# Optimization experiments

Hardware: AMD Instinct MI355X
Metric: run time of the kernel (lower is better)

Reference implementation:

```python
import jax, jax.numpy as jnp
import numpy as np

# ---- dims (match init_kwargs) ----
B0, C0, H0, W0 = 16, 64, 128, 128
G = 8            # d_model of inner Mamba2
D_STATE = 16
D_CONV = 3
EXPAND = 2
HEADDIM = 8
D_INNER = EXPAND * G            # 16
NHEADS = D_INNER // HEADDIM     # 2
NGROUPS = 1
CONV_DIM = D_INNER + 2 * NGROUPS * D_STATE   # 48
D_IN_PROJ = 2 * D_INNER + 2 * NGROUPS * D_STATE + NHEADS  # 66
EPS = 1e-5


def silu(x):
    return x * jax.nn.sigmoid(x)


def setup_inputs() -> dict:
    key = jax.random.key(0)
    ks = jax.random.split(key, 12)
    s = 0.02
    return {
        "x": jax.random.normal(ks[0], (B0, C0, H0, W0), jnp.float32),
        # 1x1 conv tokenize / detokenize (stored as matrices)
        "w_tok": jax.random.normal(ks[1], (G, C0), jnp.float32) * s,
        "b_tok": jnp.zeros((G,), jnp.float32),
        "w_detok": jax.random.normal(ks[2], (C0, G), jnp.float32) * s,
        "b_detok": jnp.zeros((C0,), jnp.float32),
        # Mamba2 params
        "w_in": jax.random.normal(ks[3], (D_IN_PROJ, G), jnp.float32) * s,
        "w_conv": jax.random.normal(ks[4], (CONV_DIM, 1, D_CONV), jnp.float32) * s,
        "b_conv": jnp.zeros((CONV_DIM,), jnp.float32),
        "dt_bias": jax.random.uniform(ks[5], (NHEADS,), jnp.float32, -4.0, -2.0),
        "A_log": jnp.log(jnp.arange(1, NHEADS + 1, dtype=jnp.float32)),
        "D": jnp.ones((NHEADS,), jnp.float32),
        "norm_w": jnp.ones((D_INNER,), jnp.float32),
        "w_out": jax.random.normal(ks[6], (G, D_INNER), jnp.float32) * s,
    }


def _mamba2(u, w_in, w_conv, b_conv, dt_bias, A_log, D, norm_w, w_out):
    # u: [B, L, G]
    Bb, L, _ = u.shape
    zxbcdt = jnp.einsum('blg,dg->bld', u, w_in)                 # [B,L,66]
    z = zxbcdt[..., :D_INNER]                                   # [B,L,16]
    xBC = zxbcdt[..., D_INNER:D_INNER + CONV_DIM]               # [B,L,48]
    dt = jax.nn.softplus(zxbcdt[..., D_INNER + CONV_DIM:] + dt_bias)  # [B,L,H]

    # causal depthwise conv1d over time
    xBC_t = jnp.moveaxis(xBC, 1, 2)                             # [B,48,L]
    xBC_t = jnp.pad(xBC_t, ((0, 0), (0, 0), (D_CONV - 1, 0)))
    xBC_t = jax.lax.conv_general_dilated(
        xBC_t, w_conv, window_strides=(1,), padding='VALID',
        dimension_numbers=('NCH', 'OIH', 'NCH'), feature_group_count=CONV_DIM)
    xBC = silu(jnp.moveaxis(xBC_t + b_conv[None, :, None], 1, 2))  # [B,L,48]

    xh = xBC[..., :D_INNER].reshape(Bb, L, NHEADS, HEADDIM)     # [B,L,H,P]
    Bm = xBC[..., D_INNER:D_INNER + D_STATE]                    # [B,L,N] (ngroups=1)
    Cm = xBC[..., D_INNER + D_STATE:]                           # [B,L,N]

    A = -jnp.exp(A_log)                                         # [H]
    dA = jnp.exp(dt * A)                                        # [B,L,H]

    # time-major sequential selective scan
    def step(state, inp):
        dA_t, dt_t, x_t, B_t, C_t = inp  # [B,H],[B,H],[B,H,P],[B,N],[B,N]
        state = state * dA_t[:, :, None, None] \
            + (dt_t[:, :, None] * x_t)[..., None] * B_t[:, None, None, :]
        y = jnp.einsum('bhpn,bn->bhp', state, C_t)
        return state, y

    init = jnp.zeros((Bb, NHEADS, HEADDIM, D_STATE), u.dtype)
    xs = (jnp.moveaxis(dA, 1, 0), jnp.moveaxis(dt, 1, 0),
          jnp.moveaxis(xh, 1, 0), jnp.moveaxis(Bm, 1, 0), jnp.moveaxis(Cm, 1, 0))
    _, ys = jax.lax.scan(step, init, xs)                        # [L,B,H,P]
    y = jnp.moveaxis(ys, 0, 1) + D[None, None, :, None] * xh    # [B,L,H,P]
    y = y.reshape(Bb, L, D_INNER)

    # gated RMSNorm then out projection
    y = y * silu(z)
    y = y * jax.lax.rsqrt(jnp.mean(y * y, axis=-1, keepdims=True) + EPS) * norm_w
    return jnp.einsum('bld,gd->blg', y, w_out)


def reference(x, w_tok, b_tok, w_detok, b_detok, w_in, w_conv, b_conv,
              dt_bias, A_log, D, norm_w, w_out):
    Bb, C, H, W = x.shape
    g = jnp.einsum('bchw,gc->bghw', x, w_tok) + b_tok[None, :, None, None]
    g = g.reshape(Bb, G, H * W).transpose(0, 2, 1)              # [B,HW,G]
    g = _mamba2(g, w_in, w_conv, b_conv, dt_bias, A_log, D, norm_w, w_out) + g
    g = g.transpose(0, 2, 1).reshape(Bb, G, H, W)
    return x + jnp.einsum('bghw,cg->bchw', g, w_detok) + b_detok[None, :, None, None]
```

## Files before the change

kernel.cpp:

```cpp
#include <hip/hip_runtime.h>

namespace {
constexpr int NB   = 16;
constexpr int NC   = 64;
constexpr int HW   = 128*128;
constexpr int SL   = 16384;
constexpr int CQ   = 64;
constexpr int NCH  = SL/CQ;
constexpr int WCH  = 4;

typedef short short8 __attribute__((ext_vector_type(8)));
typedef float f32x4  __attribute__((ext_vector_type(4)));

__device__ __forceinline__ float frcp(float x){ return __builtin_amdgcn_rcpf(x); }
__device__ __forceinline__ float rl(float v, int s){
  return __int_as_float(__builtin_amdgcn_readlane(__float_as_int(v), s));
}
__device__ __forceinline__ float sigu(float a){ return frcp(1.0f + __expf(-a)); }
__device__ __forceinline__ float softplusf(float a){
  return fmaxf(a, 0.f) + __logf(1.f + __expf(-fabsf(a)));
}
__device__ __forceinline__ unsigned bfr(float x){
  unsigned u = __float_as_uint(x);
  u = u + 0x7FFF + ((u>>16)&1);
  return u>>16;
}
__device__ __forceinline__ unsigned pk2(float a, float b){
  return (bfr(a)&0xFFFFu) | (bfr(b)<<16);
}
union CV8 { unsigned u[4]; short8 s; };

__global__ __launch_bounds__(256) void k_tok(
    const float* __restrict__ x, const float* __restrict__ w_tok,
    const float* __restrict__ b_tok, float* __restrict__ g0)
{
  __shared__ float s_wt[NC][8];
  __shared__ float s_bt[8];
  for (int i = threadIdx.x; i < NC*8; i += 256) s_wt[i>>3][i&7] = w_tok[(i&7)*NC + (i>>3)];
  if (threadIdx.x < 8) s_bt[threadIdx.x] = b_tok[threadIdx.x];
  __syncthreads();
  long idx = (long)blockIdx.x * 256 + threadIdx.x;
  int b = (int)(idx >> 14);
  int l = (int)(idx & (SL-1));
  float acc[8];
  #pragma unroll
  for (int g = 0; g < 8; ++g) acc[g] = s_bt[g];
  const float* xp = x + (long)b*NC*HW + l;
  #pragma unroll 8
  for (int c = 0; c < NC; ++c) {
    float v = xp[(long)c*HW];
    const float4* wr = (const float4*)s_wt[c];
    float4 w0 = wr[0], w1 = wr[1];
    acc[0] += v*w0.x; acc[1] += v*w0.y; acc[2] += v*w0.z; acc[3] += v*w0.w;
    acc[4] += v*w1.x; acc[5] += v*w1.y; acc[6] += v*w1.z; acc[7] += v*w1.w;
  }
  float* gp = g0 + idx*8;
  *(float4*)gp     = make_float4(acc[0],acc[1],acc[2],acc[3]);
  *(float4*)(gp+4) = make_float4(acc[4],acc[5],acc[6],acc[7]);
}

template<int PASS>
__global__ __launch_bounds__(256)
void k_chunk(
    const float* __restrict__ g0, const float* __restrict__ w_in,
    const float* __restrict__ w_conv, const float* __restrict__ b_conv,
    const float* __restrict__ dt_bias, const float* __restrict__ A_log,
    const float* __restrict__ Dvec, const float* __restrict__ norm_w,
    const float* __restrict__ w_out,
    float* __restrict__ Sc, float* __restrict__ Pc,
    const float* __restrict__ Stin, float* __restrict__ gf)
{
  constexpr int JMAX = (PASS==1) ? 48 : 32;
  constexpr int PW = (PASS==1) ? 10752 : 4096;
  __shared__ float s_win[66][8];
  __shared__ float s_wc[48][4];
  __shared__ float s_wout[8][16];
  __shared__ float s_nw[16];
  __shared__ float s_misc[8];
  __shared__ char  s_big[WCH*PW];

  int tid = threadIdx.x, lane = tid & 63, wave = tid >> 6;
  int c15 = lane & 15, lg = lane >> 4;

  for (int i = tid; i < 66*8; i += 256) s_win[i>>3][i&7] = w_in[i];
  if (tid < 48) {
    s_wc[tid][0] = w_conv[tid*3];   s_wc[tid][1] = w_conv[tid*3+1];
    s_wc[tid][2] = w_conv[tid*3+2]; s_wc[tid][3] = b_conv[tid];
  }
  if (tid < 128) s_wout[tid>>4][tid&15] = w_out[tid];
  if (tid < 16)  s_nw[tid] = norm_w[tid];
  if (tid < 2) {
    s_misc[tid]   = -__expf(A_log[tid]);
    s_misc[2+tid] = dt_bias[tid];
    s_misc[4+tid] = Dvec[tid];
  }
  __syncthreads();

  auto dot8 = [&](const float* uu, int row) -> float {
    const float4* wr = (const float4*)s_win[row];
    float4 w0 = wr[0], w1 = wr[1];
    return uu[0]*w0.x + uu[1]*w0.y + uu[2]*w0.z + uu[3]*w0.w
         + uu[4]*w1.x + uu[5]*w1.y + uu[6]*w1.z + uu[7]*w1.w;
  };

  int b   = blockIdx.x >> 6;
  int chB = (blockIdx.x & 63)*WCH + wave;
  long cg = (long)b*NCH + chB;
  int l0  = chB*CQ;
  long pos = (long)b*SL + l0 + lane;
  char* WR = &s_big[wave*PW];

  float u[8];
  { const float* up = g0 + pos*8;
    float4 a = *(const float4*)up, c = *(const float4*)(up+4);
    u[0]=a.x;u[1]=a.y;u[2]=a.z;u[3]=a.w;u[4]=c.x;u[5]=c.y;u[6]=c.z;u[7]=c.w; }

  float hA, hB = 0.f;
  {
    int pA = lane >> 5, jA = lane & 31;
    int hlA = l0 - 2 + pA;
    bool okA = (hlA >= 0);
    const float* hp2 = g0 + ((long)b*SL + (okA ? hlA : 0))*8;
    float4 a = *(const float4*)hp2, c = *(const float4*)(hp2+4);
    float uA[8] = {a.x,a.y,a.z,a.w,c.x,c.y,c.z,c.w};
    hA = okA ? dot8(uA, 16+jA) : 0.f;
    if constexpr (PASS==1) {
      int pB = (lane >> 4) & 1, jB = 32 + (lane & 15);
      int hlB = l0 - 2 + pB;
      bool okB = (hlB >= 0);
      const float* hq = g0 + ((long)b*SL + (okB ? hlB : 0))*8;
      float4 a2 = *(const float4*)hq, c2 = *(const float4*)(hq+4);
      float uB[8] = {a2.x,a2.y,a2.z,a2.w,c2.x,c2.y,c2.z,c2.w};
      hB = okB ? dot8(uB, 16+jB) : 0.f;
    }
  }

  float xv[16], Bv[16];
  float Cr[(PASS==1) ? 16 : 1];
  #pragma unroll
  for (int jb = 0; jb < JMAX/8; ++jb) {
    float pr[8];
    #pragma unroll
    for (int jj = 0; jj < 8; ++jj) pr[jj] = dot8(u, 16 + jb*8 + jj);
    #pragma unroll
    for (int jj = 0; jj < 8; ++jj) {
      int j = jb*8 + jj;
      float pm1 = __shfl_up(pr[jj], 1);
      float pm2 = __shfl_up(pr[jj], 2);
      float h0j = (j < 32) ? rl(hA, j)      : rl(hB, j-32);
      float h1j = (j < 32) ? rl(hA, 32+j)   : rl(hB, 16+(j-32));
      pm1 = (lane == 0) ? h1j : pm1;
      pm2 = (lane == 0) ? h0j : ((lane == 1) ? h1j : pm2);
      float4 wc = *(const float4*)s_wc[j];
      float a = wc.w + pm2*wc.x + pm1*wc.y + pr[jj]*wc.z;
      float s = a * sigu(a);
      if (j < 16) xv[j] = s;
      else if (j < 32) Bv[j-16] = s;
      else { if constexpr (PASS==1) Cr[j-32] = s; }
    }
  }

  float dt0 = softplusf(dot8(u, 64) + s_misc[2]);
  float dt1 = softplusf(dot8(u, 65) + s_misc[3]);
  float c0 = s_misc[0]*dt0, c1 = s_misc[1]*dt1;
  #pragma unroll
  for (int off = 1; off < 64; off <<= 1) {
    float t0 = __shfl_up(c0, off), t1 = __shfl_up(c1, off);
    if (lane >= off) { c0 += t0; c1 += t1; }
  }
  float ce0 = __expf(c0), ce1 = __expf(c1);
  float cf0 = __expf(-c0)*dt0, cf1 = __expf(-c1)*dt1;
  float cee0 = rl(ce0, 63), cee1 = rl(ce1, 63);

  char* xp = WR + ((PASS==1) ? 8192 : 2048);
  #pragma unroll
  for (int hp = 0; hp < 16; ++hp) {
    float cfh = (hp < 8) ? cf0 : cf1;
    *(short*)(xp + hp*128 + ((lane*2) ^ ((hp&7)<<4))) = (short)bfr(cfh*xv[hp]);
  }

  if constexpr (PASS==0) {
    char* BT = WR;
    #pragma unroll
    for (int n = 0; n < 16; ++n)
      *(short*)(BT + n*128 + ((lane*2) ^ ((n&7)<<4))) = (short)bfr(Bv[n]);
    __builtin_amdgcn_wave_barrier();
    __builtin_amdgcn_sched_barrier(0);
    f32x4 acc = {0.f,0.f,0.f,0.f};
    #pragma unroll
    for (int kb = 0; kb < 2; ++kb) {
      int cb = (64*kb + 16*lg) ^ ((c15&7)<<4);
      short8 Af = *(const short8*)(xp + c15*128 + cb);
      short8 Bf = *(const short8*)(BT + c15*128 + cb);
      acc = __builtin_amdgcn_mfma_f32_16x16x32_bf16(Af, Bf, acc, 0, 0, 0);
    }
    float cee = (lg < 2) ? cee0 : cee1;
    #pragma unroll
    for (int r = 0; r < 4; ++r)
      Sc[cg*256 + (4*lg+r)*16 + c15] = cee*acc[r];
    if (lane == 0) { Pc[cg*2] = cee0; Pc[cg*2+1] = cee1; }
  } else {
    char* uB  = WR;
    char* uC  = WR + 2048;
    char* Mb  = WR;
    char* ytr = WR;
    char* ceB = WR + 10240;
    { CV8 w;
      w.u[0]=pk2(Bv[0],Bv[1]);  w.u[1]=pk2(Bv[2],Bv[3]);
      w.u[2]=pk2(Bv[4],Bv[5]);  w.u[3]=pk2(Bv[6],Bv[7]);
      *(short8*)(uB + lane*32) = w.s;
      w.u[0]=pk2(Bv[8],Bv[9]);  w.u[1]=pk2(Bv[10],Bv[11]);
      w.u[2]=pk2(Bv[12],Bv[13]);w.u[3]=pk2(Bv[14],Bv[15]);
      *(short8*)(uB + lane*32 + 16) = w.s;
      w.u[0]=pk2(Cr[0],Cr[1]);  w.u[1]=pk2(Cr[2],Cr[3]);
      w.u[2]=pk2(Cr[4],Cr[5]);  w.u[3]=pk2(Cr[6],Cr[7]);
      *(short8*)(uC + lane*32) = w.s;
      w.u[0]=pk2(Cr[8],Cr[9]);  w.u[1]=pk2(Cr[10],Cr[11]);
      w.u[2]=pk2(Cr[12],Cr[13]);w.u[3]=pk2(Cr[14],Cr[15]);
      *(short8*)(uC + lane*32 + 16) = w.s;
    }
    *(float*)(ceB + lane*4)       = ce0;
    *(float*)(ceB + 256 + lane*4) = ce1;
    __builtin_amdgcn_wave_barrier();
    __builtin_amdgcn_sched_barrier(0);

    short8 zero8 = {0,0,0,0,0,0,0,0};
    f32x4  zero4 = {0.f,0.f,0.f,0.f};
    short8 Cfr[4], Bfr[4];
    #pragma unroll
    for (int tt = 0; tt < 4; ++tt) {
      Cfr[tt] = zero8; Bfr[tt] = zero8;
      if (lg < 2) {
        Cfr[tt] = *(const short8*)(uC + (16*tt + c15)*32 + 16*lg);
        Bfr[tt] = *(const short8*)(uB + (16*tt + c15)*32 + 16*lg);
      }
    }
    short8 stf = zero8;
    if (lg < 2) {
      const float* sp = Stin + cg*256 + c15*16 + 8*lg;
      float4 s0 = *(const float4*)sp, s1 = *(const float4*)(sp+4);
      CV8 cv;
      cv.u[0]=pk2(s0.x,s0.y); cv.u[1]=pk2(s0.z,s0.w);
      cv.u[2]=pk2(s1.x,s1.y); cv.u[3]=pk2(s1.z,s1.w);
      stf = cv.s;
    }
    f32x4 acc[4];
    #pragma unroll
    for (int tt = 0; tt < 4; ++tt)
      acc[tt] = __builtin_amdgcn_mfma_f32_16x16x32_bf16(Cfr[tt], stf, zero4, 0,0,0);

    #pragma unroll
    for (int tt = 0; tt < 4; ++tt) {
      int t  = 16*tt + c15;
      int sw = (t&7)<<4;
      #pragma unroll
      for (int ts = 0; ts < 4; ++ts) {
        if (ts <= tt) {
          f32x4 gA = __builtin_amdgcn_mfma_f32_16x16x32_bf16(Bfr[ts], Cfr[tt], zero4, 0,0,0);
          if (ts == tt) {
            #pragma unroll
            for (int r = 0; r < 4; ++r)
              gA[r] = (4*lg + r <= c15) ? gA[r] : 0.f;
          }
          uint2 wv; wv.x = pk2(gA[0],gA[1]); wv.y = pk2(gA[2],gA[3]);
          *(uint2*)(Mb + t*128 + ((32*ts + 8*lg) ^ sw)) = wv;
        }
      }
      if (tt == 0 || tt == 2) {
        uint2 zv; zv.x = 0u; zv.y = 0u;
        *(uint2*)(Mb + t*128 + ((32*(tt+1) + 8*lg) ^ sw)) = zv;
      }
    }
    __builtin_amdgcn_wave_barrier();
    __builtin_amdgcn_sched_barrier(0);

    short8 Xf[2];
    #pragma unroll
    for (int kb = 0; kb < 2; ++kb)
      Xf[kb] = *(const short8*)(xp + c15*128 + ((64*kb + 16*lg) ^ ((c15&7)<<4)));
    #pragma unroll
    for (int tt = 0; tt < 4; ++tt) {
      int t = 16*tt + c15, sw = (t&7)<<4;
      {
        short8 Mf = *(const short8*)(Mb + t*128 + ((16*lg) ^ sw));
        acc[tt] = __builtin_amdgcn_mfma_f32_16x16x32_bf16(Mf, Xf[0], acc[tt], 0,0,0);
      }
      if (tt >= 2) {
        short8 Mf = *(const short8*)(Mb + t*128 + ((64 + 16*lg) ^ sw));
        acc[tt] = __builtin_amdgcn_mfma_f32_16x16x32_bf16(Mf, Xf[1], acc[tt], 0,0,0);
      }
    }
    int hh = (c15 < 8) ? 0 : 1;
    #pragma unroll
    for (int tt = 0; tt < 4; ++tt) {
      float4 cev = *(const float4*)(ceB + hh*256 + (16*tt + 4*lg)*4);
      float cva[4] = {cev.x, cev.y, cev.z, cev.w};
      #pragma unroll
      for (int r = 0; r < 4; ++r)
        *(float*)(ytr + (16*tt + 4*lg + r)*96 + c15*4) = cva[r]*acc[tt][r];
    }
    __builtin_amdgcn_wave_barrier();
    __builtin_amdgcn_sched_barrier(0);

    float yr[16];
    #pragma unroll
    for (int i = 0; i < 4; ++i) {
      float4 q = *(const float4*)(ytr + lane*96 + 16*i);
      yr[4*i] = q.x; yr[4*i+1] = q.y; yr[4*i+2] = q.z; yr[4*i+3] = q.w;
    }
    float D0 = s_misc[4], D1 = s_misc[5];
    float yv[16]; float ss = 0.f;
    #pragma unroll
    for (int d = 0; d < 16; ++d) {
      float base = yr[d] + ((d < 8) ? D0 : D1)*xv[d];
      float zz = dot8(u, d);
      float v = base * (zz * sigu(zz));
      yv[d] = v; ss += v*v;
    }
    float scn = rsqrtf(ss*(1.f/16.f) + 1e-5f);
    { const float4* nw = (const float4*)s_nw;
      float4 n0 = nw[0], n1 = nw[1], n2 = nw[2], n3 = nw[3];
      yv[0]*=scn*n0.x; yv[1]*=scn*n0.y; yv[2]*=scn*n0.z; yv[3]*=scn*n0.w;
      yv[4]*=scn*n1.x; yv[5]*=scn*n1.y; yv[6]*=scn*n1.z; yv[7]*=scn*n1.w;
      yv[8]*=scn*n2.x; yv[9]*=scn*n2.y; yv[10]*=scn*n2.z; yv[11]*=scn*n2.w;
      yv[12]*=scn*n3.x; yv[13]*=scn*n3.y; yv[14]*=scn*n3.z; yv[15]*=scn*n3.w; }
    float og[8];
    #pragma unroll
    for (int g = 0; g < 8; ++g) {
      const float4* wr = (const float4*)s_wout[g];
      float4 w0 = wr[0], w1 = wr[1], w2 = wr[2], w3 = wr[3];
      float a = u[g];
      a += yv[0]*w0.x + yv[1]*w0.y + yv[2]*w0.z + yv[3]*w0.w;
      a += yv[4]*w1.x + yv[5]*w1.y + yv[6]*w1.z + yv[7]*w1.w;
      a += yv[8]*w2.x + yv[9]*w2.y + yv[10]*w2.z + yv[11]*w2.w;
      a += yv[12]*w3.x + yv[13]*w3.y + yv[14]*w3.z + yv[15]*w3.w;
      og[g] = a;
    }
    float* gp = gf + pos*8;
    *(float4*)gp     = make_float4(og[0],og[1],og[2],og[3]);
    *(float4*)(gp+4) = make_float4(og[4],og[5],og[6],og[7]);
  }
}

__global__ __launch_bounds__(256) void k_scan(
    const float* __restrict__ Sc, const float* __restrict__ Pc,
    float* __restrict__ Stin)
{
  int b = blockIdx.x;
  int tid = threadIdx.x;
  int h = tid >> 7;
  float st = 0.f;
  long base = (long)b * NCH;
  #pragma unroll 8
  for (int c = 0; c < NCH; ++c) {
    Stin[(base + c)*256 + tid] = st;
    st = st * Pc[(base + c)*2 + h] + Sc[(base + c)*256 + tid];
  }
}

__global__ __launch_bounds__(256) void k_detok(
    const float* __restrict__ x, const float* __restrict__ gf,
    const float* __restrict__ w_detok, const float* __restrict__ b_detok,
    float* __restrict__ out)
{
  __shared__ float s_wd[NC][8];
  __shared__ float s_bd[NC];
  for (int i = threadIdx.x; i < NC*8; i += 256) s_wd[i>>3][i&7] = w_detok[i];
  if (threadIdx.x < NC) s_bd[threadIdx.x] = b_detok[threadIdx.x];
  __syncthreads();
  long idx = (long)blockIdx.x * 256 + threadIdx.x;
  int b = (int)(idx >> 14);
  int l = (int)(idx & (SL-1));
  float gv[8];
  const float* gp = gf + idx*8;
  { float4 a = *(const float4*)gp, c = *(const float4*)(gp+4);
    gv[0]=a.x;gv[1]=a.y;gv[2]=a.z;gv[3]=a.w;gv[4]=c.x;gv[5]=c.y;gv[6]=c.z;gv[7]=c.w; }
  const float* xp = x + (long)b*NC*HW + l;
  float* op = out + (long)b*NC*HW + l;
  #pragma unroll 4
  for (int c = 0; c < NC; ++c) {
    const float4* wr = (const float4*)s_wd[c];
    float4 w0 = wr[0], w1 = wr[1];
    float a = s_bd[c] + xp[(long)c*HW];
    a += gv[0]*w0.x + gv[1]*w0.y + gv[2]*w0.z + gv[3]*w0.w;
    a += gv[4]*w1.x + gv[5]*w1.y + gv[6]*w1.z + gv[7]*w1.w;
    op[(long)c*HW] = a;
  }
}
}

extern "C" void kernel_launch(void* const* d_in, const int* in_sizes, int n_in,
                              void* d_out, int out_size, void* d_ws, size_t ws_size,
                              hipStream_t stream)
{
  const float* x       = (const float*)d_in[0];
  const float* w_tok   = (const float*)d_in[1];
  const float* b_tok   = (const float*)d_in[2];
  const float* w_detok = (const float*)d_in[3];
  const float* b_detok = (const float*)d_in[4];
  const float* w_in    = (const float*)d_in[5];
  const float* w_conv  = (const float*)d_in[6];
  const float* b_conv  = (const float*)d_in[7];
  const float* dt_bias = (const float*)d_in[8];
  const float* A_log   = (const float*)d_in[9];
  const float* Dvec    = (const float*)d_in[10];
  const float* norm_w  = (const float*)d_in[11];
  const float* w_out   = (const float*)d_in[12];
  float* out = (float*)d_out;

  float* ws   = (float*)d_ws;
  float* g0   = ws;
  float* gf   = g0 + (long)NB*SL*8;
  float* Sc   = gf + (long)NB*SL*8;
  float* Pc   = Sc + (long)NB*NCH*256;
  float* Stin = Pc + (long)NB*NCH*2;

  k_tok<<<NB*SL/256, 256, 0, stream>>>(x, w_tok, b_tok, g0);
  k_chunk<0><<<NB*NCH/WCH, 256, 0, stream>>>(g0, w_in, w_conv, b_conv, dt_bias,
                                             A_log, Dvec, norm_w, w_out,
                                             Sc, Pc, nullptr, nullptr);
  k_scan<<<NB, 256, 0, stream>>>(Sc, Pc, Stin);
  k_chunk<1><<<NB*NCH/WCH, 256, 0, stream>>>(g0, w_in, w_conv, b_conv, dt_bias,
                                             A_log, Dvec, norm_w, w_out,
                                             Sc, Pc, Stin, gf);
  k_detok<<<NB*SL/256, 256, 0, stream>>>(x, gf, w_detok, b_detok, out);
}
```

Before: 106.5 us.

## Split chunk pass into front (intra-chunk) and light apply kernel after scan

Instead of recomputing in_proj, conv, the decay cumsum and the intra-chunk MFMA work in two passes, one front kernel now does all of it once. It writes the chunk states, the decay factors, the C values as bf16 and the partial intra-chunk outputs to global workspace. After the inter-chunk scan, a new apply kernel reads these back, adds the C·state contribution in scalar FP32, then does the gating, RMSNorm and out projection. This removes the duplicated front-end compute but adds extra global traffic for the intermediates (Yg, Cg, ceg) and runs the front kernel with 2-wave blocks.

Result: slower. 121.0 us (+13.6%).

```diff
diff --git a/kernel.cpp b/kernel.cpp
--- a/kernel.cpp
+++ b/kernel.cpp
@@ -7,7 +7,6 @@
 constexpr int SL   = 16384;
 constexpr int CQ   = 64;
 constexpr int NCH  = SL/CQ;
-constexpr int WCH  = 4;
 
 typedef short short8 __attribute__((ext_vector_type(8)));
 typedef float f32x4  __attribute__((ext_vector_type(4)));
@@ -28,6 +27,8 @@
 __device__ __forceinline__ unsigned pk2(float a, float b){
   return (bfr(a)&0xFFFFu) | (bfr(b)<<16);
 }
+__device__ __forceinline__ float blo(unsigned u){ return __uint_as_float(u<<16); }
+__device__ __forceinline__ float bhi(unsigned u){ return __uint_as_float(u & 0xFFFF0000u); }
 union CV8 { unsigned u[4]; short8 s; };
 
 __global__ __launch_bounds__(256) void k_tok(
@@ -59,36 +60,28 @@
   *(float4*)(gp+4) = make_float4(acc[4],acc[5],acc[6],acc[7]);
 }
 
-template<int PASS>
-__global__ __launch_bounds__(256)
-void k_chunk(
+__global__ __launch_bounds__(128) void k_front(
     const float* __restrict__ g0, const float* __restrict__ w_in,
     const float* __restrict__ w_conv, const float* __restrict__ b_conv,
     const float* __restrict__ dt_bias, const float* __restrict__ A_log,
-    const float* __restrict__ Dvec, const float* __restrict__ norm_w,
-    const float* __restrict__ w_out,
+    const float* __restrict__ Dvec,
     float* __restrict__ Sc, float* __restrict__ Pc,
-    const float* __restrict__ Stin, float* __restrict__ gf)
-{
-  constexpr int JMAX = (PASS==1) ? 48 : 32;
-  constexpr int PW = (PASS==1) ? 10752 : 4096;
+    float* __restrict__ ceg, unsigned short* __restrict__ Cg,
+    float* __restrict__ Yg)
+{
   __shared__ float s_win[66][8];
   __shared__ float s_wc[48][4];
-  __shared__ float s_wout[8][16];
-  __shared__ float s_nw[16];
   __shared__ float s_misc[8];
-  __shared__ char  s_big[WCH*PW];
+  __shared__ char  s_big[2*10240];
 
   int tid = threadIdx.x, lane = tid & 63, wave = tid >> 6;
   int c15 = lane & 15, lg = lane >> 4;
 
-  for (int i = tid; i < 66*8; i += 256) s_win[i>>3][i&7] = w_in[i];
+  for (int i = tid; i < 66*8; i += 128) s_win[i>>3][i&7] = w_in[i];
   if (tid < 48) {
     s_wc[tid][0] = w_conv[tid*3];   s_wc[tid][1] = w_conv[tid*3+1];
     s_wc[tid][2] = w_conv[tid*3+2]; s_wc[tid][3] = b_conv[tid];
   }
-  if (tid < 128) s_wout[tid>>4][tid&15] = w_out[tid];
-  if (tid < 16)  s_nw[tid] = norm_w[tid];
   if (tid < 2) {
     s_misc[tid]   = -__expf(A_log[tid]);
     s_misc[2+tid] = dt_bias[tid];
@@ -103,12 +96,18 @@
          + uu[4]*w1.x + uu[5]*w1.y + uu[6]*w1.z + uu[7]*w1.w;
   };
 
-  int b   = blockIdx.x >> 6;
-  int chB = (blockIdx.x & 63)*WCH + wave;
+  int b   = blockIdx.x >> 7;
+  int chB = (blockIdx.x & 127)*2 + wave;
   long cg = (long)b*NCH + chB;
   int l0  = chB*CQ;
   long pos = (long)b*SL + l0 + lane;
-  char* WR = &s_big[wave*PW];
+  char* WR = &s_big[wave*10240];
+  char* xp = WR;
+  char* Mb = WR + 2048;
+  char* BT = Mb;
+  char* uB = Mb + 2048;
+  char* uC = Mb + 4096;
+  char* ceB = xp;
 
   float u[8];
   { const float* up = g0 + pos*8;
@@ -124,21 +123,18 @@
     float4 a = *(const float4*)hp2, c = *(const float4*)(hp2+4);
     float uA[8] = {a.x,a.y,a.z,a.w,c.x,c.y,c.z,c.w};
     hA = okA ? dot8(uA, 16+jA) : 0.f;
-    if constexpr (PASS==1) {
-      int pB = (lane >> 4) & 1, jB = 32 + (lane & 15);
-      int hlB = l0 - 2 + pB;
-      bool okB = (hlB >= 0);
-      const float* hq = g0 + ((long)b*SL + (okB ? hlB : 0))*8;
-      float4 a2 = *(const float4*)hq, c2 = *(const float4*)(hq+4);
-      float uB[8] = {a2.x,a2.y,a2.z,a2.w,c2.x,c2.y,c2.z,c2.w};
-      hB = okB ? dot8(uB, 16+jB) : 0.f;
-    }
-  }
-
-  float xv[16], Bv[16];
-  float Cr[(PASS==1) ? 16 : 1];
-  #pragma unroll
-  for (int jb = 0; jb < JMAX/8; ++jb) {
+    int pB = (lane >> 4) & 1, jB = 32 + (lane & 15);
+    int hlB = l0 - 2 + pB;
+    bool okB = (hlB >= 0);
+    const float* hq = g0 + ((long)b*SL + (okB ? hlB : 0))*8;
+    float4 a2 = *(const float4*)hq, c2 = *(const float4*)(hq+4);
+    float uB8[8] = {a2.x,a2.y,a2.z,a2.w,c2.x,c2.y,c2.z,c2.w};
+    hB = okB ? dot8(uB8, 16+jB) : 0.f;
+  }
+
+  float xv[16], Bv[16], Cr[16];
+  #pragma unroll
+  for (int jb = 0; jb < 6; ++jb) {
     float pr[8];
     #pragma unroll
     for (int jj = 0; jj < 8; ++jj) pr[jj] = dot8(u, 16 + jb*8 + jj);
@@ -156,7 +152,7 @@
       float s = a * sigu(a);
       if (j < 16) xv[j] = s;
       else if (j < 32) Bv[j-16] = s;
-      else { if constexpr (PASS==1) Cr[j-32] = s; }
+      else Cr[j-32] = s;
     }
   }
 
@@ -172,174 +168,143 @@
   float cf0 = __expf(-c0)*dt0, cf1 = __expf(-c1)*dt1;
   float cee0 = rl(ce0, 63), cee1 = rl(ce1, 63);
 
-  char* xp = WR + ((PASS==1) ? 8192 : 2048);
+  ceg[cg*128 + lane]      = ce0;
+  ceg[cg*128 + 64 + lane] = ce1;
+  { CV8 w;
+    w.u[0]=pk2(Cr[0],Cr[1]);  w.u[1]=pk2(Cr[2],Cr[3]);
+    w.u[2]=pk2(Cr[4],Cr[5]);  w.u[3]=pk2(Cr[6],Cr[7]);
+    *(short8*)(Cg + cg*1024 + lane*16) = w.s;
+    w.u[0]=pk2(Cr[8],Cr[9]);  w.u[1]=pk2(Cr[10],Cr[11]);
+    w.u[2]=pk2(Cr[12],Cr[13]);w.u[3]=pk2(Cr[14],Cr[15]);
+    *(short8*)(Cg + cg*1024 + lane*16 + 8) = w.s;
+  }
+  if (lane == 0) { Pc[cg*2] = cee0; Pc[cg*2+1] = cee1; }
+
   #pragma unroll
   for (int hp = 0; hp < 16; ++hp) {
     float cfh = (hp < 8) ? cf0 : cf1;
     *(short*)(xp + hp*128 + ((lane*2) ^ ((hp&7)<<4))) = (short)bfr(cfh*xv[hp]);
   }
-
-  if constexpr (PASS==0) {
-    char* BT = WR;
-    #pragma unroll
-    for (int n = 0; n < 16; ++n)
-      *(short*)(BT + n*128 + ((lane*2) ^ ((n&7)<<4))) = (short)bfr(Bv[n]);
-    __builtin_amdgcn_wave_barrier();
-    __builtin_amdgcn_sched_barrier(0);
-    f32x4 acc = {0.f,0.f,0.f,0.f};
+  #pragma unroll
+  for (int n = 0; n < 16; ++n)
+    *(short*)(BT + n*128 + ((lane*2) ^ ((n&7)<<4))) = (short)bfr(Bv[n]);
+  { CV8 w;
+    w.u[0]=pk2(Bv[0],Bv[1]);  w.u[1]=pk2(Bv[2],Bv[3]);
+    w.u[2]=pk2(Bv[4],Bv[5]);  w.u[3]=pk2(Bv[6],Bv[7]);
+    *(short8*)(uB + lane*32) = w.s;
+    w.u[0]=pk2(Bv[8],Bv[9]);  w.u[1]=pk2(Bv[10],Bv[11]);
+    w.u[2]=pk2(Bv[12],Bv[13]);w.u[3]=pk2(Bv[14],Bv[15]);
+    *(short8*)(uB + lane*32 + 16) = w.s;
+    w.u[0]=pk2(Cr[0],Cr[1]);  w.u[1]=pk2(Cr[2],Cr[3]);
+    w.u[2]=pk2(Cr[4],Cr[5]);  w.u[3]=pk2(Cr[6],Cr[7]);
+    *(short8*)(uC + lane*32) = w.s;
+    w.u[0]=pk2(Cr[8],Cr[9]);  w.u[1]=pk2(Cr[10],Cr[11]);
+    w.u[2]=pk2(Cr[12],Cr[13]);w.u[3]=pk2(Cr[14],Cr[15]);
+    *(short8*)(uC + lane*32 + 16) = w.s;
+  }
+  __builtin_amdgcn_wave_barrier();
+  __builtin_amdgcn_sched_barrier(0x7F);
+
+  short8 zero8 = {0,0,0,0,0,0,0,0};
+  f32x4  zero4 = {0.f,0.f,0.f,0.f};
+  { f32x4 sacc = zero4;
     #pragma unroll
     for (int kb = 0; kb < 2; ++kb) {
       int cb = (64*kb + 16*lg) ^ ((c15&7)<<4);
       short8 Af = *(const short8*)(xp + c15*128 + cb);
       short8 Bf = *(const short8*)(BT + c15*128 + cb);
-      acc = __builtin_amdgcn_mfma_f32_16x16x32_bf16(Af, Bf, acc, 0, 0, 0);
+      sacc = __builtin_amdgcn_mfma_f32_16x16x32_bf16(Af, Bf, sacc, 0, 0, 0);
     }
     float cee = (lg < 2) ? cee0 : cee1;
     #pragma unroll
     for (int r = 0; r < 4; ++r)
-      Sc[cg*256 + (4*lg+r)*16 + c15] = cee*acc[r];
-    if (lane == 0) { Pc[cg*2] = cee0; Pc[cg*2+1] = cee1; }
-  } else {
-    char* uB  = WR;
-    char* uC  = WR + 2048;
-    char* Mb  = WR;
-    char* ytr = WR;
-    char* ceB = WR + 10240;
-    { CV8 w;
-      w.u[0]=pk2(Bv[0],Bv[1]);  w.u[1]=pk2(Bv[2],Bv[3]);
-      w.u[2]=pk2(Bv[4],Bv[5]);  w.u[3]=pk2(Bv[6],Bv[7]);
-      *(short8*)(uB + lane*32) = w.s;
-      w.u[0]=pk2(Bv[8],Bv[9]);  w.u[1]=pk2(Bv[10],Bv[11]);
-      w.u[2]=pk2(Bv[12],Bv[13]);w.u[3]=pk2(Bv[14],Bv[15]);
-      *(short8*)(uB + lane*32 + 16) = w.s;
-      w.u[0]=pk2(Cr[0],Cr[1]);  w.u[1]=pk2(Cr[2],Cr[3]);
-      w.u[2]=pk2(Cr[4],Cr[5]);  w.u[3]=pk2(Cr[6],Cr[7]);
-      *(short8*)(uC + lane*32) = w.s;
-      w.u[0]=pk2(Cr[8],Cr[9]);  w.u[1]=pk2(Cr[10],Cr[11]);
-      w.u[2]=pk2(Cr[12],Cr[13]);w.u[3]=pk2(Cr[14],Cr[15]);
-      *(short8*)(uC + lane*32 + 16) = w.s;
-    }
-    *(float*)(ceB + lane*4)       = ce0;
-    *(float*)(ceB + 256 + lane*4) = ce1;
-    __builtin_amdgcn_wave_barrier();
-    __builtin_amdgcn_sched_barrier(0);
-
-    short8 zero8 = {0,0,0,0,0,0,0,0};
-    f32x4  zero4 = {0.f,0.f,0.f,0.f};
-    short8 Cfr[4], Bfr[4];
-    #pragma unroll
-    for (int tt = 0; tt < 4; ++tt) {
-      Cfr[tt] = zero8; Bfr[tt] = zero8;
-      if (lg < 2) {
-        Cfr[tt] = *(const short8*)(uC + (16*tt + c15)*32 + 16*lg);
-        Bfr[tt] = *(const short8*)(uB + (16*tt + c15)*32 + 16*lg);
+      Sc[cg*256 + (4*lg+r)*16 + c15] = cee*sacc[r];
+  }
+
+  short8 Cfr[4], Bfr[4], Xf[2];
+  #pragma unroll
+  for (int tt = 0; tt < 4; ++tt) {
+    Cfr[tt] = zero8; Bfr[tt] = zero8;
+    if (lg < 2) {
+      Cfr[tt] = *(const short8*)(uC + (16*tt + c15)*32 + 16*lg);
+      Bfr[tt] = *(const short8*)(uB + (16*tt + c15)*32 + 16*lg);
+    }
+  }
+  #pragma unroll
+  for (int kb = 0; kb < 2; ++kb)
+    Xf[kb] = *(const short8*)(xp + c15*128 + ((64*kb + 16*lg) ^ ((c15&7)<<4)));
+  __builtin_amdgcn_wave_barrier();
+  __builtin_amdgcn_sched_barrier(0x7F);
+
+  #pragma unroll
+  for (int tt = 0; tt < 4; ++tt) {
+    int t  = 16*tt + c15;
+    int sw = (t&7)<<4;
+    #pragma unroll
+    for (int ts = 0; ts < 4; ++ts) {
+      if (ts <= tt) {
+        f32x4 gA = __builtin_amdgcn_mfma_f32_16x16x32_bf16(Bfr[ts], Cfr[tt], zero4, 0,0,0);
+        if (ts == tt) {
+          #pragma unroll
+          for (int r = 0; r < 4; ++r)
+            gA[r] = (4*lg + r <= c15) ? gA[r] : 0.f;
+        }
+        uint2 wv; wv.x = pk2(gA[0],gA[1]); wv.y = pk2(gA[2],gA[3]);
+        *(uint2*)(Mb + t*128 + ((32*ts + 8*lg) ^ sw)) = wv;
       }
     }
-    short8 stf = zero8;
-    if (lg < 2) {
-      const float* sp = Stin + cg*256 + c15*16 + 8*lg;
-      float4 s0 = *(const float4*)sp, s1 = *(const float4*)(sp+4);
-      CV8 cv;
-      cv.u[0]=pk2(s0.x,s0.y); cv.u[1]=pk2(s0.z,s0.w);
-      cv.u[2]=pk2(s1.x,s1.y); cv.u[3]=pk2(s1.z,s1.w);
-      stf = cv.s;
-    }
-    f32x4 acc[4];
-    #pragma unroll
-    for (int tt = 0; tt < 4; ++tt)
-      acc[tt] = __builtin_amdgcn_mfma_f32_16x16x32_bf16(Cfr[tt], stf, zero4, 0,0,0);
-
-    #pragma unroll
-    for (int tt = 0; tt < 4; ++tt) {
-      int t  = 16*tt + c15;
-      int sw = (t&7)<<4;
-      #pragma unroll
-      for (int ts = 0; ts < 4; ++ts) {
-        if (ts <= tt) {
-          f32x4 gA = __builtin_amdgcn_mfma_f32_16x16x32_bf16(Bfr[ts], Cfr[tt], zero4, 0,0,0);
-          if (ts == tt) {
-            #pragma unroll
-            for (int r = 0; r < 4; ++r)
-              gA[r] = (4*lg + r <= c15) ? gA[r] : 0.f;
-          }
-          uint2 wv; wv.x = pk2(gA[0],gA[1]); wv.y = pk2(gA[2],gA[3]);
-          *(uint2*)(Mb + t*128 + ((32*ts + 8*lg) ^ sw)) = wv;
-        }
-      }
-      if (tt == 0 || tt == 2) {
-        uint2 zv; zv.x = 0u; zv.y = 0u;
-        *(uint2*)(Mb + t*128 + ((32*(tt+1) + 8*lg) ^ sw)) = zv;
-      }
-    }
-    __builtin_amdgcn_wave_barrier();
-    __builtin_amdgcn_sched_barrier(0);
-
-    short8 Xf[2];
-    #pragma unroll
-    for (int kb = 0; kb < 2; ++kb)
-      Xf[kb] = *(const short8*)(xp + c15*128 + ((64*kb + 16*lg) ^ ((c15&7)<<4)));
-    #pragma unroll
-    for (int tt = 0; tt < 4; ++tt) {
-      int t = 16*tt + c15, sw = (t&7)<<4;
-      {
-        short8 Mf = *(const short8*)(Mb + t*128 + ((16*lg) ^ sw));
-        acc[tt] = __builtin_amdgcn_mfma_f32_16x16x32_bf16(Mf, Xf[0], acc[tt], 0,0,0);
-      }
-      if (tt >= 2) {
-        short8 Mf = *(const short8*)(Mb + t*128 + ((64 + 16*lg) ^ sw));
-        acc[tt] = __builtin_amdgcn_mfma_f32_16x16x32_bf16(Mf, Xf[1], acc[tt], 0,0,0);
-      }
-    }
-    int hh = (c15 < 8) ? 0 : 1;
-    #pragma unroll
-    for (int tt = 0; tt < 4; ++tt) {
-      float4 cev = *(const float4*)(ceB + hh*256 + (16*tt + 4*lg)*4);
-      float cva[4] = {cev.x, cev.y, cev.z, cev.w};
-      #pragma unroll
-      for (int r = 0; r < 4; ++r)
-        *(float*)(ytr + (16*tt + 4*lg + r)*96 + c15*4) = cva[r]*acc[tt][r];
-    }
-    __builtin_amdgcn_wave_barrier();
-    __builtin_amdgcn_sched_barrier(0);
-
-    float yr[16];
-    #pragma unroll
-    for (int i = 0; i < 4; ++i) {
-      float4 q = *(const float4*)(ytr + lane*96 + 16*i);
-      yr[4*i] = q.x; yr[4*i+1] = q.y; yr[4*i+2] = q.z; yr[4*i+3] = q.w;
-    }
-    float D0 = s_misc[4], D1 = s_misc[5];
-    float yv[16]; float ss = 0.f;
-    #pragma unroll
-    for (int d = 0; d < 16; ++d) {
-      float base = yr[d] + ((d < 8) ? D0 : D1)*xv[d];
-      float zz = dot8(u, d);
-      float v = base * (zz * sigu(zz));
-      yv[d] = v; ss += v*v;
-    }
-    float scn = rsqrtf(ss*(1.f/16.f) + 1e-5f);
-    { const float4* nw = (const float4*)s_nw;
-      float4 n0 = nw[0], n1 = nw[1], n2 = nw[2], n3 = nw[3];
-      yv[0]*=scn*n0.x; yv[1]*=scn*n0.y; yv[2]*=scn*n0.z; yv[3]*=scn*n0.w;
-      yv[4]*=scn*n1.x; yv[5]*=scn*n1.y; yv[6]*=scn*n1.z; yv[7]*=scn*n1.w;
-      yv[8]*=scn*n2.x; yv[9]*=scn*n2.y; yv[10]*=scn*n2.z; yv[11]*=scn*n2.w;
-      yv[12]*=scn*n3.x; yv[13]*=scn*n3.y; yv[14]*=scn*n3.z; yv[15]*=scn*n3.w; }
-    float og[8];
-    #pragma unroll
-    for (int g = 0; g < 8; ++g) {
-      const float4* wr = (const float4*)s_wout[g];
-      float4 w0 = wr[0], w1 = wr[1], w2 = wr[2], w3 = wr[3];
-      float a = u[g];
-      a += yv[0]*w0.x + yv[1]*w0.y + yv[2]*w0.z + yv[3]*w0.w;
-      a += yv[4]*w1.x + yv[5]*w1.y + yv[6]*w1.z + yv[7]*w1.w;
-      a += yv[8]*w2.x + yv[9]*w2.y + yv[10]*w2.z + yv[11]*w2.w;
-      a += yv[12]*w3.x + yv[13]*w3.y + yv[14]*w3.z + yv[15]*w3.w;
-      og[g] = a;
-    }
-    float* gp = gf + pos*8;
-    *(float4*)gp     = make_float4(og[0],og[1],og[2],og[3]);
-    *(float4*)(gp+4) = make_float4(og[4],og[5],og[6],og[7]);
-  }
+    if (tt == 0 || tt == 2) {
+      uint2 zv; zv.x = 0u; zv.y = 0u;
+      *(uint2*)(Mb + t*128 + ((32*(tt+1) + 8*lg) ^ sw)) = zv;
+    }
+  }
+  *(float*)(ceB + lane*4)       = ce0;
+  *(float*)(ceB + 256 + lane*4) = ce1;
+  __builtin_amdgcn_wave_barrier();
+  __builtin_amdgcn_sched_barrier(0x7F);
+
+  f32x4 acc[4];
+  #pragma unroll
+  for (int tt = 0; tt < 4; ++tt) acc[tt] = zero4;
+  #pragma unroll
+  for (int tt = 0; tt < 4; ++tt) {
+    int t = 16*tt + c15, sw = (t&7)<<4;
+    {
+      short8 Mf = *(const short8*)(Mb + t*128 + ((16*lg) ^ sw));
+      acc[tt] = __builtin_amdgcn_mfma_f32_16x16x32_bf16(Mf, Xf[0], acc[tt], 0,0,0);
+    }
+    if (tt >= 2) {
+      short8 Mf = *(const short8*)(Mb + t*128 + ((64 + 16*lg) ^ sw));
+      acc[tt] = __builtin_amdgcn_mfma_f32_16x16x32_bf16(Mf, Xf[1], acc[tt], 0,0,0);
+    }
+  }
+  char* ytr = Mb;
+  int hh = (c15 < 8) ? 0 : 1;
+  #pragma unroll
+  for (int tt = 0; tt < 4; ++tt) {
+    float4 cev = *(const float4*)(ceB + hh*256 + (16*tt + 4*lg)*4);
+    float cva[4] = {cev.x, cev.y, cev.z, cev.w};
+    #pragma unroll
+    for (int r = 0; r < 4; ++r)
+      *(float*)(ytr + (16*tt + 4*lg + r)*96 + c15*4) = cva[r]*acc[tt][r];
+  }
+  __builtin_amdgcn_wave_barrier();
+  __builtin_amdgcn_sched_barrier(0x7F);
+
+  float D0 = s_misc[4], D1 = s_misc[5];
+  float yr[16];
+  #pragma unroll
+  for (int i = 0; i < 4; ++i) {
+    float4 q = *(const float4*)(ytr + lane*96 + 16*i);
+    yr[4*i] = q.x; yr[4*i+1] = q.y; yr[4*i+2] = q.z; yr[4*i+3] = q.w;
+  }
+  #pragma unroll
+  for (int d = 0; d < 16; ++d) yr[d] += ((d < 8) ? D0 : D1)*xv[d];
+  float* yg = Yg + cg*1024 + lane*16;
+  *(float4*)(yg)    = make_float4(yr[0],yr[1],yr[2],yr[3]);
+  *(float4*)(yg+4)  = make_float4(yr[4],yr[5],yr[6],yr[7]);
+  *(float4*)(yg+8)  = make_float4(yr[8],yr[9],yr[10],yr[11]);
+  *(float4*)(yg+12) = make_float4(yr[12],yr[13],yr[14],yr[15]);
 }
 
 __global__ __launch_bounds__(256) void k_scan(
@@ -356,6 +321,109 @@
     Stin[(base + c)*256 + tid] = st;
     st = st * Pc[(base + c)*2 + h] + Sc[(base + c)*256 + tid];
   }
+}
+
+__global__ __launch_bounds__(256) void k_apply(
+    const float* __restrict__ g0, const float* __restrict__ w_in,
+    const float* __restrict__ norm_w, const float* __restrict__ w_out,
+    const float* __restrict__ Stin, const float* __restrict__ ceg,
+    const unsigned short* __restrict__ Cg, const float* __restrict__ Yg,
+    float* __restrict__ gf)
+{
+  __shared__ float s_win[16][8];
+  __shared__ float s_wout[8][16];
+  __shared__ float s_nw[16];
+  __shared__ float s_st[4][256];
+
+  int tid = threadIdx.x, lane = tid & 63, wave = tid >> 6;
+  if (tid < 128) s_win[tid>>3][tid&7] = w_in[tid];
+  if (tid < 128) s_wout[tid>>4][tid&15] = w_out[tid];
+  if (tid < 16)  s_nw[tid] = norm_w[tid];
+  __syncthreads();
+
+  auto dot8 = [&](const float* uu, int row) -> float {
+    const float4* wr = (const float4*)s_win[row];
+    float4 w0 = wr[0], w1 = wr[1];
+    return uu[0]*w0.x + uu[1]*w0.y + uu[2]*w0.z + uu[3]*w0.w
+         + uu[4]*w1.x + uu[5]*w1.y + uu[6]*w1.z + uu[7]*w1.w;
+  };
+
+  int b   = blockIdx.x >> 6;
+  int chB = (blockIdx.x & 63)*4 + wave;
+  long cg = (long)b*NCH + chB;
+  long pos = (long)b*SL + chB*CQ + lane;
+
+  { float4 t4 = *(const float4*)(Stin + cg*256 + lane*4);
+    *(float4*)&s_st[wave][lane*4] = t4; }
+
+  float u[8];
+  { const float* up = g0 + pos*8;
+    float4 a = *(const float4*)up, c = *(const float4*)(up+4);
+    u[0]=a.x;u[1]=a.y;u[2]=a.z;u[3]=a.w;u[4]=c.x;u[5]=c.y;u[6]=c.z;u[7]=c.w; }
+
+  float Cr[16];
+  { const uint4* cp = (const uint4*)(Cg + cg*1024 + lane*16);
+    uint4 ca = cp[0], cb = cp[1];
+    Cr[0]=blo(ca.x); Cr[1]=bhi(ca.x); Cr[2]=blo(ca.y); Cr[3]=bhi(ca.y);
+    Cr[4]=blo(ca.z); Cr[5]=bhi(ca.z); Cr[6]=blo(ca.w); Cr[7]=bhi(ca.w);
+    Cr[8]=blo(cb.x); Cr[9]=bhi(cb.x); Cr[10]=blo(cb.y); Cr[11]=bhi(cb.y);
+    Cr[12]=blo(cb.z); Cr[13]=bhi(cb.z); Cr[14]=blo(cb.w); Cr[15]=bhi(cb.w); }
+
+  float yr[16];
+  { const float* yp = Yg + cg*1024 + lane*16;
+    #pragma unroll
+    for (int i = 0; i < 4; ++i) {
+      float4 q = *(const float4*)(yp + 4*i);
+      yr[4*i]=q.x; yr[4*i+1]=q.y; yr[4*i+2]=q.z; yr[4*i+3]=q.w;
+    } }
+  float ce0t = ceg[cg*128 + lane];
+  float ce1t = ceg[cg*128 + 64 + lane];
+
+  __builtin_amdgcn_wave_barrier();
+  __builtin_amdgcn_sched_barrier(0x7F);
+
+  const float* st = &s_st[wave][0];
+  float y[16];
+  #pragma unroll
+  for (int hp = 0; hp < 16; ++hp) {
+    const float4* sp = (const float4*)(st + hp*16);
+    float4 s0 = sp[0], s1 = sp[1], s2 = sp[2], s3 = sp[3];
+    float a = Cr[0]*s0.x + Cr[1]*s0.y + Cr[2]*s0.z + Cr[3]*s0.w
+            + Cr[4]*s1.x + Cr[5]*s1.y + Cr[6]*s1.z + Cr[7]*s1.w
+            + Cr[8]*s2.x + Cr[9]*s2.y + Cr[10]*s2.z + Cr[11]*s2.w
+            + Cr[12]*s3.x + Cr[13]*s3.y + Cr[14]*s3.z + Cr[15]*s3.w;
+    y[hp] = yr[hp] + ((hp < 8) ? ce0t : ce1t)*a;
+  }
+
+  float yv[16]; float ss = 0.f;
+  #pragma unroll
+  for (int d = 0; d < 16; ++d) {
+    float zz = dot8(u, d);
+    float v = y[d] * (zz * sigu(zz));
+    yv[d] = v; ss += v*v;
+  }
+  float scn = rsqrtf(ss*(1.f/16.f) + 1e-5f);
+  { const float4* nw = (const float4*)s_nw;
+    float4 n0 = nw[0], n1 = nw[1], n2 = nw[2], n3 = nw[3];
+    yv[0]*=scn*n0.x; yv[1]*=scn*n0.y; yv[2]*=scn*n0.z; yv[3]*=scn*n0.w;
+    yv[4]*=scn*n1.x; yv[5]*=scn*n1.y; yv[6]*=scn*n1.z; yv[7]*=scn*n1.w;
+    yv[8]*=scn*n2.x; yv[9]*=scn*n2.y; yv[10]*=scn*n2.z; yv[11]*=scn*n2.w;
+    yv[12]*=scn*n3.x; yv[13]*=scn*n3.y; yv[14]*=scn*n3.z; yv[15]*=scn*n3.w; }
+  float og[8];
+  #pragma unroll
+  for (int g = 0; g < 8; ++g) {
+    const float4* wr = (const float4*)s_wout[g];
+    float4 w0 = wr[0], w1 = wr[1], w2 = wr[2], w3 = wr[3];
+    float a = u[g];
+    a += yv[0]*w0.x + yv[1]*w0.y + yv[2]*w0.z + yv[3]*w0.w;
+    a += yv[4]*w1.x + yv[5]*w1.y + yv[6]*w1.z + yv[7]*w1.w;
+    a += yv[8]*w2.x + yv[9]*w2.y + yv[10]*w2.z + yv[11]*w2.w;
+    a += yv[12]*w3.x + yv[13]*w3.y + yv[14]*w3.z + yv[15]*w3.w;
+    og[g] = a;
+  }
+  float* gp = gf + pos*8;
+  *(float4*)gp     = make_float4(og[0],og[1],og[2],og[3]);
+  *(float4*)(gp+4) = make_float4(og[4],og[5],og[6],og[7]);
 }
 
 __global__ __launch_bounds__(256) void k_detok(
@@ -414,14 +482,15 @@
   float* Sc   = gf + (long)NB*SL*8;
   float* Pc   = Sc + (long)NB*NCH*256;
   float* Stin = Pc + (long)NB*NCH*2;
+  float* ceg  = Stin + (long)NB*NCH*256;
+  float* Yg   = ceg + (long)NB*NCH*128;
+  unsigned short* Cg = (unsigned short*)(Yg + (long)NB*NCH*1024);
 
   k_tok<<<NB*SL/256, 256, 0, stream>>>(x, w_tok, b_tok, g0);
-  k_chunk<0><<<NB*NCH/WCH, 256, 0, stream>>>(g0, w_in, w_conv, b_conv, dt_bias,
-                                             A_log, Dvec, norm_w, w_out,
-                                             Sc, Pc, nullptr, nullptr);
+  k_front<<<NB*NCH/2, 128, 0, stream>>>(g0, w_in, w_conv, b_conv, dt_bias,
+                                        A_log, Dvec, Sc, Pc, ceg, Cg, Yg);
   k_scan<<<NB, 256, 0, stream>>>(Sc, Pc, Stin);
-  k_chunk<1><<<NB*NCH/WCH, 256, 0, stream>>>(g0, w_in, w_conv, b_conv, dt_bias,
-                                             A_log, Dvec, norm_w, w_out,
-                                             Sc, Pc, Stin, gf);
+  k_apply<<<NB*NCH/4, 256, 0, stream>>>(g0, w_in, norm_w, w_out,
+                                        Stin, ceg, Cg, Yg, gf);
   k_detok<<<NB*SL/256, 256, 0, stream>>>(x, gf, w_detok, b_detok, out);
 }
```
